# Kernel tuning notes

Hardware: AMD Instinct MI355X
Metric: run time of the kernel (lower is better)

## Reference

```python
import jax, jax.numpy as jnp
import numpy as np

H = 4      # SSM / attn heads (d_model/headdim = 256/64)
WIN = 4    # attention window over bands


def _ln(x, g, b):
    m = jnp.mean(x, -1, keepdims=True)
    v = jnp.mean((x - m) ** 2, -1, keepdims=True)
    return (x - m) * jax.lax.rsqrt(v + 1e-5) * g + b


def setup_inputs() -> dict:
    key = jax.random.key(0)
    ks = jax.random.split(key, 24)
    def rn(i, shape, s=0.05):
        return jax.random.normal(ks[i], shape, jnp.float32) * s
    B, T, K, D = 2, 256, 8, 256
    return {
        "z": rn(0, (B, T, K, D), 1.0),
        "ln1_g": jnp.ones((D,), jnp.float32), "ln1_b": jnp.zeros((D,), jnp.float32),
        "Wx": rn(1, (D, D)), "conv_w": rn(2, (D, 4), 0.3), "Wz": rn(3, (D, D)),
        "Wb": rn(4, (D, H * 128)), "Wc": rn(5, (D, H * 128)), "Wdt": rn(6, (D, H)),
        "dt_bias": rn(7, (H,), 0.5), "A_log": rn(8, (H,), 0.5), "theta": rn(9, (H,), 1.0),
        "D_skip": rn(10, (H,), 1.0), "mimo_U": rn(11, (H, H), 0.5), "mimo_V": rn(12, (H, H), 0.5),
        "Wout": rn(13, (D, D)),
        "ln2_g": jnp.ones((D,), jnp.float32), "ln2_b": jnp.zeros((D,), jnp.float32),
        "attn_in_w": rn(14, (3 * D, D)), "attn_in_b": rn(15, (3 * D,), 0.02),
        "attn_out_w": rn(16, (D, D)), "attn_out_b": jnp.zeros((D,), jnp.float32),
        "ln3_g": jnp.ones((D,), jnp.float32), "ln3_b": jnp.zeros((D,), jnp.float32),
        "Wg": rn(17, (D, 4 * D)), "Wu": rn(18, (D, 4 * D)), "Wd": rn(19, (4 * D, D)),
    }


def _forward(z, ln1_g, ln1_b, Wx, conv_w, Wz, Wb, Wc, Wdt, dt_bias, A_log, theta,
             D_skip, mimo_U, mimo_V, Wout, ln2_g, ln2_b, attn_in_w, attn_in_b,
             attn_out_w, attn_out_b, ln3_g, ln3_b, Wg, Wu, Wd):
    B, T, K, D = z.shape
    P = D // H
    N = Wb.shape[1] // H
    # ---------- (a) intra-band Mamba3 (complex MIMO selective scan) ----------
    u = _ln(z, ln1_g, ln1_b)
    u = jnp.transpose(u, (0, 2, 1, 3)).reshape(B * K, T, D)   # [BK,T,D]
    x = u @ Wx
    # causal depthwise conv1d, kernel 4
    xp = jnp.pad(x, ((0, 0), (3, 0), (0, 0)))
    x = sum(xp[:, k:k + T, :] * conv_w[:, k] for k in range(4))
    x = jax.nn.silu(x)
    xh = x.reshape(B * K, T, H, P)
    Bm = (u @ Wb).reshape(B * K, T, H, N)
    Cm = (u @ Wc).reshape(B * K, T, H, N)
    Mmix = mimo_U @ mimo_V.T                                  # rank-r cross-head coupling
    Bm = jnp.einsum('hg,btgn->bthn', Mmix, Bm)
    dt = jax.nn.softplus(u @ Wdt + dt_bias)                   # [BK,T,H]
    A = -jnp.exp(A_log)                                       # stable real decay
    mag = jnp.exp(dt * A)
    ph = dt * theta                                           # harmonic rotation
    ar, ai = mag * jnp.cos(ph), mag * jnp.sin(ph)
    xs = tuple(jnp.moveaxis(t, 1, 0) for t in (xh, Bm, Cm, dt, ar, ai))
    h0 = jnp.zeros((B * K, H, N, P), x.dtype)

    def step(carry, s):
        h_re, h_im = carry
        xt, bt, ct, dtt, art, ait = s
        dBx = (dtt[:, :, None, None] * bt[:, :, :, None]) * xt[:, :, None, :]
        nr = art[:, :, None, None] * h_re - ait[:, :, None, None] * h_im + dBx
        ni = art[:, :, None, None] * h_im + ait[:, :, None, None] * h_re
        return (nr, ni), jnp.einsum('bhn,bhnp->bhp', ct, nr)   # Re(C . h)

    _, ys = jax.lax.scan(step, (h0, h0), xs)                  # ys: [T,BK,H,P]
    y = jnp.moveaxis(ys, 0, 1) + D_skip[None, None, :, None] * xh
    y = y.reshape(B * K, T, D) * jax.nn.silu(u @ Wz)
    y = y @ Wout
    z = z + jnp.transpose(y.reshape(B, K, T, D), (0, 2, 1, 3))
    # ---------- (b) inter-band windowed attention ----------
    zn = _ln(z, ln2_g, ln2_b).reshape(B * T, K, D)
    qkv = zn @ attn_in_w.T + attn_in_b
    q, k_, v = jnp.split(qkv, 3, axis=-1)
    hd = D // H
    def hs(t):
        return t.reshape(B * T, K // WIN, WIN, H, hd).transpose(0, 1, 3, 2, 4)
    q, k_, v = hs(q), hs(k_), hs(v)
    s = jnp.einsum('mwhqd,mwhkd->mwhqk', q, k_) * jnp.float32(1.0 / np.sqrt(hd))
    a = jax.nn.softmax(s, axis=-1)
    o = jnp.einsum('mwhqk,mwhkd->mwhqd', a, v).transpose(0, 1, 3, 2, 4).reshape(B * T, K, D)
    z = z + (o @ attn_out_w.T + attn_out_b).reshape(B, T, K, D)
    # ---------- (c) SwiGLU FFN ----------
    zf = _ln(z, ln3_g, ln3_b)
    z = z + (jax.nn.silu(zf @ Wg) * (zf @ Wu)) @ Wd
    return z


def reference(z, ln1_g, ln1_b, Wx, conv_w, Wz, Wb, Wc, Wdt, dt_bias, A_log, theta,
              D_skip, mimo_U, mimo_V, Wout, ln2_g, ln2_b, attn_in_w, attn_in_b,
              attn_out_w, attn_out_b, ln3_g, ln3_b, Wg, Wu, Wd):
    return _forward(z, ln1_g, ln1_b, Wx, conv_w, Wz, Wb, Wc, Wdt, dt_bias, A_log,
                    theta, D_skip, mimo_U, mimo_V, Wout, ln2_g, ln2_b, attn_in_w,
                    attn_in_b, attn_out_w, attn_out_b, ln3_g, ln3_b, Wg, Wu, Wd)
```

## Files before the change

### kernel.cpp

```cpp
#include <hip/hip_runtime.h>
#include <hip/hip_bf16.h>
#include <math.h>

typedef __hip_bfloat16 bf16;
typedef __attribute__((ext_vector_type(8))) short s16x8;
typedef __attribute__((ext_vector_type(4))) float f32x4;

__device__ __forceinline__ float siluf(float x) { return x / (1.f + __expf(-x)); }
__device__ __forceinline__ float bits2f(unsigned short u) {
    union { float f; unsigned i; } v; v.i = ((unsigned)u) << 16; return v.f;
}
__device__ __forceinline__ unsigned short f2bits(float f) {
    return (unsigned short)__bfloat16_as_ushort(__float2bfloat16(f));
}

#define KFL 1024
#define OFF_UB   (768*KFL)
#define OFF_DTV  (1280*KFL)
#define OFF_BMB  (1344*KFL)
#define OFF_CMB  (2368*KFL)
#define OFF_ZGB  (3392*KFL)
#define OFF_XB   (3904*KFL)
#define OFF_X2T  (4928*KFL)
#define OFF_P    (5440*KFL)
#define OFF_YGB  (7488*KFL)
#define OFF_Z2   (8000*KFL)
#define OFF_ZFB  (9024*KFL)
#define OFF_GG   OFF_BMB

#define W_BCZX 0
#define W_OUT  393216
#define W_QKV  458752
#define W_AO   655360
#define W_GU   720896
#define W_D    1245184

__global__ __launch_bounds__(256) void prep_ln1_kernel(
    const float* __restrict__ Wx, const float* __restrict__ Wb,
    const float* __restrict__ Wc, const float* __restrict__ Wz,
    const float* __restrict__ Wo, const float* __restrict__ Wqkv,
    const float* __restrict__ Wao, const float* __restrict__ Wg,
    const float* __restrict__ Wu, const float* __restrict__ Wd,
    const float* __restrict__ U, const float* __restrict__ V,
    unsigned short* __restrict__ wout,
    const float* __restrict__ z, const float* __restrict__ g1,
    const float* __restrict__ b1, const float* __restrict__ Wdt,
    const float* __restrict__ dt_bias,
    unsigned short* __restrict__ u, float4* __restrict__ dtv4)
{
    __shared__ __align__(16) float smem[64 * 65];
    int blk = blockIdx.x;
    int tid = threadIdx.x;
    if (blk < 368) {
        if (blk >= 304) {
            int off = blk - 304;
            const float* src; int dst, base;
            if (off < 48) { src = Wqkv; dst = W_QKV; base = off * 4096; }
            else          { src = Wao;  dst = W_AO;  base = (off - 48) * 4096; }
            #pragma unroll
            for (int i = 0; i < 16; i++) {
                int idx = base + tid + i * 256;
                wout[dst + idx] = f2bits(src[idx]);
            }
            return;
        }
        float* lds = smem;
        const float* src; int srcN, n0, sc0, k0, dstoff, dstK, mix = 0, t;
        if (blk < 32)       { t = blk;       src = Wb; srcN = 512;  dstoff = W_BCZX; dstK = 256;
                              n0 = (t >> 2) * 64;        sc0 = 0; k0 = (t & 3) * 64; mix = 1; }
        else if (blk < 64)  { t = blk - 32;  src = Wc; srcN = 512;  dstoff = W_BCZX; dstK = 256;
                              n0 = 512 + (t >> 2) * 64;  sc0 = (t >> 2) * 64; k0 = (t & 3) * 64; }
        else if (blk < 80)  { t = blk - 64;  src = Wz; srcN = 256;  dstoff = W_BCZX; dstK = 256;
                              n0 = 1024 + (t >> 2) * 64; sc0 = (t >> 2) * 64; k0 = (t & 3) * 64; }
        else if (blk < 96)  { t = blk - 80;  src = Wx; srcN = 256;  dstoff = W_BCZX; dstK = 256;
                              n0 = 1280 + (t >> 2) * 64; sc0 = (t >> 2) * 64; k0 = (t & 3) * 64; }
        else if (blk < 112) { t = blk - 96;  src = Wo; srcN = 256;  dstoff = W_OUT;  dstK = 256;
                              n0 = (t >> 2) * 64;        sc0 = n0; k0 = (t & 3) * 64; }
        else if (blk < 176) { t = blk - 112; src = Wg; srcN = 1024; dstoff = W_GU;   dstK = 256;
                              n0 = (t >> 2) * 64;        sc0 = n0; k0 = (t & 3) * 64; }
        else if (blk < 240) { t = blk - 176; src = Wu; srcN = 1024; dstoff = W_GU;   dstK = 256;
                              n0 = 1024 + (t >> 2) * 64; sc0 = (t >> 2) * 64; k0 = (t & 3) * 64; }
        else                { t = blk - 240; src = Wd; srcN = 256;  dstoff = W_D;    dstK = 1024;
                              n0 = (t >> 4) * 64;        sc0 = n0; k0 = (t & 15) * 64; }
        if (mix) {
            int h = n0 >> 7, scol = n0 & 127;
            float mm[4];
            #pragma unroll
            for (int g = 0; g < 4; g++) {
                float s = 0.f;
                #pragma unroll
                for (int j = 0; j < 4; j++) s += U[h * 4 + j] * V[g * 4 + j];
                mm[g] = s;
            }
            #pragma unroll
            for (int i = 0; i < 16; i++) {
                int idx = tid + i * 256;
                int kk = idx >> 6, nn = idx & 63;
                const float* row = src + (size_t)(k0 + kk) * 512 + scol + nn;
                lds[kk * 65 + nn] = mm[0] * row[0] + mm[1] * row[128]
                                  + mm[2] * row[256] + mm[3] * row[384];
            }
        } else {
            #pragma unroll
            for (int i = 0; i < 16; i++) {
                int idx = tid + i * 256;
                int kk = idx >> 6, nn = idx & 63;
                lds[kk * 65 + nn] = src[(size_t)(k0 + kk) * srcN + sc0 + nn];
            }
        }
        __syncthreads();
        #pragma unroll
        for (int i = 0; i < 16; i++) {
            int idx = tid + i * 256;
            int nn = idx >> 6, kk = idx & 63;
            wout[dstoff + (size_t)(n0 + nn) * dstK + k0 + kk] = f2bits(lds[kk * 65 + nn]);
        }
        return;
    }
    int r = blk - 368;
    float* lds = smem;
    float* dts = smem + 4;
    int t = r & 255, bk = r >> 8;
    int b_ = bk >> 3, k = bk & 7;
    int srcr = ((b_ * 256 + t) * 8 + k) * 256;
    int d = tid;
    float x = z[srcr + d];
    float v = x;
    #pragma unroll
    for (int off = 32; off; off >>= 1) v += __shfl_xor(v, off, 64);
    if ((d & 63) == 0) lds[d >> 6] = v;
    __syncthreads();
    float mean = (lds[0] + lds[1] + lds[2] + lds[3]) * (1.f / 256.f);
    __syncthreads();
    float c = x - mean;
    v = c * c;
    #pragma unroll
    for (int off = 32; off; off >>= 1) v += __shfl_xor(v, off, 64);
    if ((d & 63) == 0) lds[d >> 6] = v;
    __syncthreads();
    float var = (lds[0] + lds[1] + lds[2] + lds[3]) * (1.f / 256.f);
    float uval = c * rsqrtf(var + 1e-5f) * g1[d] + b1[d];
    u[r * 256 + d] = f2bits(uval);
    float4 wv = *(const float4*)(Wdt + d * 4);
    float q0 = uval * wv.x, q1 = uval * wv.y, q2 = uval * wv.z, q3 = uval * wv.w;
    #pragma unroll
    for (int off = 32; off; off >>= 1) {
        q0 += __shfl_xor(q0, off, 64);
        q1 += __shfl_xor(q1, off, 64);
        q2 += __shfl_xor(q2, off, 64);
        q3 += __shfl_xor(q3, off, 64);
    }
    if ((d & 63) == 0) {
        int w = d >> 6;
        dts[w * 4 + 0] = q0; dts[w * 4 + 1] = q1;
        dts[w * 4 + 2] = q2; dts[w * 4 + 3] = q3;
    }
    __syncthreads();
    if (d == 0) {
        float dv[4];
        #pragma unroll
        for (int h = 0; h < 4; h++) {
            float xx = dts[h] + dts[4 + h] + dts[8 + h] + dts[12 + h] + dt_bias[h];
            dv[h] = (xx > 20.f) ? xx : log1pf(__expf(xx));
        }
        dtv4[r] = make_float4(dv[0], dv[1], dv[2], dv[3]);
    }
}

__global__ __launch_bounds__(256) void gemm_bczx(
    const unsigned short* __restrict__ A, const unsigned short* __restrict__ Bt,
    unsigned short* __restrict__ bmb, unsigned short* __restrict__ cmb,
    unsigned short* __restrict__ zgb, unsigned short* __restrict__ xb)
{
    __shared__ __align__(16) unsigned short As[128 * 72];
    __shared__ __align__(16) unsigned short Bs[128 * 72];
    const int K = 256;
    int tid = threadIdx.x;
    int n0 = blockIdx.x * 128, m0 = blockIdx.y * 128;
    int w = tid >> 6, l = tid & 63;
    int mwave = (w >> 1) * 64, nwave = (w & 1) * 64;
    f32x4 acc[4][4] = {};
    int srow = tid >> 3, sc = (tid & 7) * 8;
    const unsigned short* Ap = A + (size_t)(m0 + srow) * K + sc;
    const unsigned short* Bp = Bt + (size_t)(n0 + srow) * K + sc;
    int lq = l & 15, lh = l >> 4;
    uint4 a0 = *(const uint4*)(Ap);
    uint4 a1 = *(const uint4*)(Ap + (size_t)32 * K);
    uint4 a2 = *(const uint4*)(Ap + (size_t)64 * K);
    uint4 a3 = *(const uint4*)(Ap + (size_t)96 * K);
    uint4 b0 = *(const uint4*)(Bp);
    uint4 b1 = *(const uint4*)(Bp + (size_t)32 * K);
    uint4 b2 = *(const uint4*)(Bp + (size_t)64 * K);
    uint4 b3 = *(const uint4*)(Bp + (size_t)96 * K);
    for (int k0 = 0; k0 < K; k0 += 64) {
        if (k0) __syncthreads();
        *(uint4*)&As[srow * 72 + sc] = a0;
        *(uint4*)&As[(srow + 32) * 72 + sc] = a1;
        *(uint4*)&As[(srow + 64) * 72 + sc] = a2;
        *(uint4*)&As[(srow + 96) * 72 + sc] = a3;
        *(uint4*)&Bs[srow * 72 + sc] = b0;
        *(uint4*)&Bs[(srow + 32) * 72 + sc] = b1;
        *(uint4*)&Bs[(srow + 64) * 72 + sc] = b2;
        *(uint4*)&Bs[(srow + 96) * 72 + sc] = b3;
        __syncthreads();
        if (k0 + 64 < K) {
            a0 = *(const uint4*)(Ap + k0 + 64);
            a1 = *(const uint4*)(Ap + (size_t)32 * K + k0 + 64);
            a2 = *(const uint4*)(Ap + (size_t)64 * K + k0 + 64);
            a3 = *(const uint4*)(Ap + (size_t)96 * K + k0 + 64);
            b0 = *(const uint4*)(Bp + k0 + 64);
            b1 = *(const uint4*)(Bp + (size_t)32 * K + k0 + 64);
            b2 = *(const uint4*)(Bp + (size_t)64 * K + k0 + 64);
            b3 = *(const uint4*)(Bp + (size_t)96 * K + k0 + 64);
        }
        #pragma unroll
        for (int kk = 0; kk < 2; kk++) {
            int kof = kk * 32 + lh * 8;
            s16x8 bfr[4];
            #pragma unroll
            for (int nf = 0; nf < 4; nf++)
                bfr[nf] = *(const s16x8*)&Bs[(nwave + nf * 16 + lq) * 72 + kof];
            #pragma unroll
            for (int mf = 0; mf < 4; mf++) {
                s16x8 af = *(const s16x8*)&As[(mwave + mf * 16 + lq) * 72 + kof];
                #pragma unroll
                for (int nf = 0; nf < 4; nf++)
                    acc[mf][nf] = __builtin_amdgcn_mfma_f32_16x16x32_bf16(af, bfr[nf], acc[mf][nf], 0, 0, 0);
            }
        }
    }
    #pragma unroll
    for (int mf = 0; mf < 4; mf++) {
        #pragma unroll
        for (int nf = 0; nf < 4; nf++) {
            int n = n0 + nwave + nf * 16 + lq;
            #pragma unroll
            for (int r = 0; r < 4; r++) {
                int m = m0 + mwave + mf * 16 + (l >> 4) * 4 + r;
                float v = acc[mf][nf][r];
                if (n < 512)       bmb[(size_t)m * 512 + n] = f2bits(v);
                else if (n < 1024) cmb[(size_t)m * 512 + (n - 512)] = f2bits(v);
                else if (n < 1280) zgb[(size_t)m * 256 + (n - 1024)] = f2bits(siluf(v));
                else               xb[(size_t)m * 256 + (n - 1280)] = f2bits(v);
            }
        }
    }
}

__global__ __launch_bounds__(256) void s_conv_kernel(
    const unsigned short* __restrict__ cmb, const unsigned short* __restrict__ bmb,
    const float4* __restrict__ dtv4, const float* __restrict__ A_log,
    const float* __restrict__ theta, unsigned short* __restrict__ P,
    const unsigned short* __restrict__ xb, const float* __restrict__ cw,
    unsigned short* __restrict__ x2t)
{
    __shared__ __align__(16) char smem[39936];
    int blk = blockIdx.x;
    int tid = threadIdx.x;
    if (blk >= 192) {
        int c = blk - 192;
        int bhid = c >> 2, tt = c & 3;
        int bk = bhid >> 2, h = bhid & 3;
        int t0 = tt * 64;
        float* tile = (float*)smem;
        #pragma unroll
        for (int i = 0; i < 17; i++) {
            int idx = tid + i * 256;
            if (idx < 67 * 64) {
                int tr = idx >> 6, dd = idx & 63;
                int t = t0 - 3 + tr;
                tile[tr * 65 + dd] = (t >= 0)
                    ? bits2f(xb[(size_t)(bk * 256 + t) * 256 + h * 64 + dd]) : 0.f;
            }
        }
        __syncthreads();
        int wv_ = tid >> 6, lt = tid & 63;
        #pragma unroll 4
        for (int pi = 0; pi < 16; pi++) {
            int p = wv_ * 16 + pi;
            float4 wv = *(const float4*)(cw + (h * 64 + p) * 4);
            float acc = tile[lt * 65 + p] * wv.x + tile[(lt + 1) * 65 + p] * wv.y +
                        tile[(lt + 2) * 65 + p] * wv.z + tile[(lt + 3) * 65 + p] * wv.w;
            x2t[(size_t)(bhid * 64 + p) * 256 + t0 + lt] = f2bits(siluf(acc));
        }
        return;
    }
    int map = blk >> 6;
    int bh = blk & 63;
    int bx = (map == 2) ? 1 : 0;
    int by = (map == 0) ? 0 : 1;
    int bk = bh >> 2, h = bh & 3;
    unsigned short* As = (unsigned short*)smem;
    unsigned short* Bs = As + 128 * 72;
    float* mAs = (float*)(smem + 36864);
    float* phs = mAs + 256;
    float* dss = phs + 256;
    int srow = tid >> 3, sc = (tid & 7) * 8;
    const unsigned short* Ap = cmb + (size_t)(bk * 256 + by * 128 + srow) * 512 + h * 128 + sc;
    const unsigned short* Bp = bmb + (size_t)(bk * 256 + bx * 128 + srow) * 512 + h * 128 + sc;
    uint4 a0 = *(const uint4*)(Ap);
    uint4 a1 = *(const uint4*)(Ap + (size_t)32 * 512);
    uint4 a2 = *(const uint4*)(Ap + (size_t)64 * 512);
    uint4 a3 = *(const uint4*)(Ap + (size_t)96 * 512);
    uint4 b0 = *(const uint4*)(Bp);
    uint4 b1 = *(const uint4*)(Bp + (size_t)32 * 512);
    uint4 b2 = *(const uint4*)(Bp + (size_t)64 * 512);
    uint4 b3 = *(const uint4*)(Bp + (size_t)96 * 512);
    {
        float4 dv = dtv4[bk * 256 + tid];
        float dth = (h == 0) ? dv.x : (h == 1) ? dv.y : (h == 2) ? dv.z : dv.w;
        float Ah = -__expf(A_log[h]);
        float th = theta[h];
        dss[tid] = dth;
        mAs[tid] = dth * Ah;
        phs[tid] = dth * th;
        __syncthreads();
        for (int off = 1; off < 256; off <<= 1) {
            float a = 0.f, p = 0.f;
            int use = (tid >= off);
            if (use) { a = mAs[tid - off]; p = phs[tid - off]; }
            __syncthreads();
            if (use) { mAs[tid] += a; phs[tid] += p; }
            __syncthreads();
        }
    }
    int w = tid >> 6, l = tid & 63;
    int mwave = (w >> 1) * 64, nwave = (w & 1) * 64;
    int lq = l & 15, lh = l >> 4;
    unsigned short* Pout = P + (size_t)bh * 65536;
    f32x4 acc[4][4] = {};
    for (int k0 = 0; k0 < 128; k0 += 64) {
        __syncthreads();
        *(uint4*)&As[srow * 72 + sc] = a0;
        *(uint4*)&As[(srow + 32) * 72 + sc] = a1;
        *(uint4*)&As[(srow + 64) * 72 + sc] = a2;
        *(uint4*)&As[(srow + 96) * 72 + sc] = a3;
        *(uint4*)&Bs[srow * 72 + sc] = b0;
        *(uint4*)&Bs[(srow + 32) * 72 + sc] = b1;
        *(uint4*)&Bs[(srow + 64) * 72 + sc] = b2;
        *(uint4*)&Bs[(srow + 96) * 72 + sc] = b3;
        __syncthreads();
        if (k0 + 64 < 128) {
            a0 = *(const uint4*)(Ap + k0 + 64);
            a1 = *(const uint4*)(Ap + (size_t)32 * 512 + k0 + 64);
            a2 = *(const uint4*)(Ap + (size_t)64 * 512 + k0 + 64);
            a3 = *(const uint4*)(Ap + (size_t)96 * 512 + k0 + 64);
            b0 = *(const uint4*)(Bp + k0 + 64);
            b1 = *(const uint4*)(Bp + (size_t)32 * 512 + k0 + 64);
            b2 = *(const uint4*)(Bp + (size_t)64 * 512 + k0 + 64);
            b3 = *(const uint4*)(Bp + (size_t)96 * 512 + k0 + 64);
        }
        #pragma unroll
        for (int kk = 0; kk < 2; kk++) {
            int kof = kk * 32 + lh * 8;
            s16x8 bfr[4];
            #pragma unroll
            for (int nf = 0; nf < 4; nf++)
                bfr[nf] = *(const s16x8*)&Bs[(nwave + nf * 16 + lq) * 72 + kof];
            #pragma unroll
            for (int mf = 0; mf < 4; mf++) {
                s16x8 af = *(const s16x8*)&As[(mwave + mf * 16 + lq) * 72 + kof];
                #pragma unroll
                for (int nf = 0; nf < 4; nf++)
                    acc[mf][nf] = __builtin_amdgcn_mfma_f32_16x16x32_bf16(af, bfr[nf], acc[mf][nf], 0, 0, 0);
            }
        }
    }
    #pragma unroll
    for (int mf = 0; mf < 4; mf++) {
        float tmv[4], tpv[4]; int tg[4];
        #pragma unroll
        for (int r = 0; r < 4; r++) {
            tg[r] = by * 128 + mwave + mf * 16 + lh * 4 + r;
            tmv[r] = mAs[tg[r]];
            tpv[r] = phs[tg[r]];
        }
        #pragma unroll
        for (int nf = 0; nf < 4; nf++) {
            int s = bx * 128 + nwave + nf * 16 + lq;
            float ms = mAs[s];
            float ps = phs[s];
            float ds = dss[s];
            #pragma unroll
            for (int r = 0; r < 4; r++) {
                float wgt = (s <= tg[r])
                    ? __expf(tmv[r] - ms) * __cosf(tpv[r] - ps) * ds : 0.f;
                Pout[tg[r] * 256 + s] = f2bits(acc[mf][nf][r] * wgt);
            }
        }
    }
}

__global__ __launch_bounds__(256) void gemm_y(
    const unsigned short* __restrict__ P, const unsigned short* __restrict__ x2t,
    const unsigned short* __restrict__ zgb, const float* __restrict__ Dsk,
    unsigned short* __restrict__ ygb)
{
    int by = blockIdx.x, bh = blockIdx.y;
    int bk = bh >> 2, h = bh & 3;
    int tid = threadIdx.x;
    int w = tid >> 6, l = tid & 63;
    int mw = (w >> 1) * 32, nw = (w & 1) * 32;
    int lq = l & 15, lh = l >> 4;
    __shared__ __align__(16) unsigned short As[64 * 72];
    __shared__ __align__(16) unsigned short Bs[64 * 72];
    f32x4 acc[2][2] = {};
    int srow = tid >> 3, sc = (tid & 7) * 8;
    const unsigned short* Ap = P + (size_t)bh * 65536 + (size_t)(by * 64 + srow) * 256 + sc;
    const unsigned short* Bp = x2t + (size_t)bh * 16384 + (size_t)srow * 256 + sc;
    int kmax = (by + 1) * 64; if (kmax > 256) kmax = 256;
    uint4 a0 = *(const uint4*)(Ap);
    uint4 a1 = *(const uint4*)(Ap + (size_t)32 * 256);
    uint4 b0 = *(const uint4*)(Bp);
    uint4 b1 = *(const uint4*)(Bp + (size_t)32 * 256);
    for (int k0 = 0; k0 < kmax; k0 += 64) {
        if (k0) __syncthreads();
        *(uint4*)&As[srow * 72 + sc] = a0;
        *(uint4*)&As[(srow + 32) * 72 + sc] = a1;
        *(uint4*)&Bs[srow * 72 + sc] = b0;
        *(uint4*)&Bs[(srow + 32) * 72 + sc] = b1;
        __syncthreads();
        if (k0 + 64 < kmax) {
            a0 = *(const uint4*)(Ap + k0 + 64);
            a1 = *(const uint4*)(Ap + (size_t)32 * 256 + k0 + 64);
            b0 = *(const uint4*)(Bp + k0 + 64);
            b1 = *(const uint4*)(Bp + (size_t)32 * 256 + k0 + 64);
        }
        #pragma unroll
        for (int kk = 0; kk < 2; kk++) {
            int kof = kk * 32 + lh * 8;
            s16x8 bfr[2];
            #pragma unroll
            for (int nf = 0; nf < 2; nf++)
                bfr[nf] = *(const s16x8*)&Bs[(nw + nf * 16 + lq) * 72 + kof];
            #pragma unroll
            for (int mf = 0; mf < 2; mf++) {
                s16x8 af = *(const s16x8*)&As[(mw + mf * 16 + lq) * 72 + kof];
                #pragma unroll
                for (int nf = 0; nf < 2; nf++)
                    acc[mf][nf] = __builtin_amdgcn_mfma_f32_16x16x32_bf16(af, bfr[nf], acc[mf][nf], 0, 0, 0);
            }
        }
    }
    float dsk = Dsk[h];
    #pragma unroll
    for (int mf = 0; mf < 2; mf++) {
        #pragma unroll
        for (int nf = 0; nf < 2; nf++) {
            int p = nw + nf * 16 + lq;
            #pragma unroll
            for (int r = 0; r < 4; r++) {
                int t = by * 64 + mw + mf * 16 + lh * 4 + r;
                float xv = bits2f(x2t[(size_t)bh * 16384 + p * 256 + t]);
                float zg = bits2f(zgb[(size_t)(bk * 256 + t) * 256 + h * 64 + p]);
                ygb[(size_t)(bk * 256 + t) * 256 + h * 64 + p] =
                    f2bits((acc[mf][nf][r] + dsk * xv) * zg);
            }
        }
    }
}

__global__ __launch_bounds__(256) void mid_kernel(
    const unsigned short* __restrict__ ygb, const unsigned short* __restrict__ wts,
    const float* __restrict__ zin,
    const float* __restrict__ g2, const float* __restrict__ b2,
    const float* __restrict__ qbias, const float* __restrict__ obias,
    const float* __restrict__ g3, const float* __restrict__ b3,
    float* __restrict__ z2, unsigned short* __restrict__ zfb)
{
    __shared__ __align__(16) char smem[64512];
    unsigned short* Bs = (unsigned short*)smem;
    unsigned short* As = (unsigned short*)(smem + 36864);
    unsigned short* zn = (unsigned short*)(smem + 39168);
    float* z1s = (float*)(smem + 47616);
    float (*partS)[4] = (float(*)[4])(smem + 64000);
    float (*partQ)[4] = (float(*)[4])(smem + 64256);
    unsigned short* qk = (unsigned short*)smem;

    const int K = 256;
    int tid = threadIdx.x;
    int m0 = blockIdx.x * 16;
    int w = tid >> 6, l = tid & 63;
    int nw = w * 64;
    int lq = l & 15, lh = l >> 4;
    int srow = tid >> 3, sc = (tid & 7) * 8;

    {
        int rb = m0 + (srow & 15);
        int irow = ((rb >> 11) * 8 + (rb & 7)) * 256 + ((rb >> 3) & 255);
        const unsigned short* Ap = ygb + (size_t)irow * K + sc;
        const unsigned short* Bp = wts + W_OUT + (size_t)srow * K + sc;
        f32x4 acc[4] = {};
        uint4 a0 = *(const uint4*)(Ap);
        uint4 c0 = *(const uint4*)(Bp);
        uint4 c1 = *(const uint4*)(Bp + (size_t)32 * K);
        uint4 c2 = *(const uint4*)(Bp + (size_t)64 * K);
        uint4 c3 = *(const uint4*)(Bp + (size_t)96 * K);
        uint4 c4 = *(const uint4*)(Bp + (size_t)128 * K);
        uint4 c5 = *(const uint4*)(Bp + (size_t)160 * K);
        uint4 c6 = *(const uint4*)(Bp + (size_t)192 * K);
        uint4 c7 = *(const uint4*)(Bp + (size_t)224 * K);
        for (int k0 = 0; k0 < K; k0 += 64) {
            if (k0) __syncthreads();
            if (tid < 128) *(uint4*)&As[srow * 72 + sc] = a0;
            *(uint4*)&Bs[srow * 72 + sc] = c0;
            *(uint4*)&Bs[(srow + 32) * 72 + sc] = c1;
            *(uint4*)&Bs[(srow + 64) * 72 + sc] = c2;
            *(uint4*)&Bs[(srow + 96) * 72 + sc] = c3;
            *(uint4*)&Bs[(srow + 128) * 72 + sc] = c4;
            *(uint4*)&Bs[(srow + 160) * 72 + sc] = c5;
            *(uint4*)&Bs[(srow + 192) * 72 + sc] = c6;
            *(uint4*)&Bs[(srow + 224) * 72 + sc] = c7;
            __syncthreads();
            if (k0 + 64 < K) {
                a0 = *(const uint4*)(Ap + k0 + 64);
                c0 = *(const uint4*)(Bp + k0 + 64);
                c1 = *(const uint4*)(Bp + (size_t)32 * K + k0 + 64);
                c2 = *(const uint4*)(Bp + (size_t)64 * K + k0 + 64);
                c3 = *(const uint4*)(Bp + (size_t)96 * K + k0 + 64);
                c4 = *(const uint4*)(Bp + (size_t)128 * K + k0 + 64);
                c5 = *(const uint4*)(Bp + (size_t)160 * K + k0 + 64);
                c6 = *(const uint4*)(Bp + (size_t)192 * K + k0 + 64);
                c7 = *(const uint4*)(Bp + (size_t)224 * K + k0 + 64);
            }
            #pragma unroll
            for (int kk = 0; kk < 2; kk++) {
                int kof = kk * 32 + lh * 8;
                s16x8 af = *(const s16x8*)&As[lq * 72 + kof];
                #pragma unroll
                for (int nf = 0; nf < 4; nf++) {
                    s16x8 bf = *(const s16x8*)&Bs[(nw + nf * 16 + lq) * 72 + kof];
                    acc[nf] = __builtin_amdgcn_mfma_f32_16x16x32_bf16(af, bf, acc[nf], 0, 0, 0);
                }
            }
        }
        #pragma unroll
        for (int r = 0; r < 4; r++) {
            int row = lh * 4 + r;
            float s = 0.f, q = 0.f;
            #pragma unroll
            for (int nf = 0; nf < 4; nf++) {
                float v = acc[nf][r] + zin[(size_t)(m0 + row) * 256 + nw + nf * 16 + lq];
                acc[nf][r] = v;
                s += v; q += v * v;
            }
            #pragma unroll
            for (int off = 1; off < 16; off <<= 1) {
                s += __shfl_xor(s, off, 64);
                q += __shfl_xor(q, off, 64);
            }
            if (lq == 0) { partS[row][w] = s; partQ[row][w] = q; }
        }
        __syncthreads();
        float gv[4], bbv[4];
        #pragma unroll
        for (int nf = 0; nf < 4; nf++) {
            gv[nf] = g2[nw + nf * 16 + lq];
            bbv[nf] = b2[nw + nf * 16 + lq];
        }
        #pragma unroll
        for (int r = 0; r < 4; r++) {
            int row = lh * 4 + r;
            float sum = partS[row][0] + partS[row][1] + partS[row][2] + partS[row][3];
            float sq  = partQ[row][0] + partQ[row][1] + partQ[row][2] + partQ[row][3];
            float mean = sum * (1.f / 256.f);
            float var = sq * (1.f / 256.f) - mean * mean;
            float rstd = rsqrtf(var + 1e-5f);
            #pragma unroll
            for (int nf = 0; nf < 4; nf++) {
                int n = nw + nf * 16 + lq;
                float v = acc[nf][r];
                z1s[row * 256 + n] = v;
                zn[row * 264 + n] = f2bits((v - mean) * rstd * gv[nf] + bbv[nf]);
            }
        }
    }

    f32x4 aq0[4] = {}, aq1[4] = {}, aq2[4] = {};
#define QKV_PASS(PIDX, AQ) do { \
    const unsigned short* Bp2 = wts + W_QKV + (size_t)((PIDX) * 256 + srow) * 256 + sc; \
    uint4 d0 = *(const uint4*)(Bp2); \
    uint4 d1 = *(const uint4*)(Bp2 + (size_t)32 * 256); \
    uint4 d2 = *(const uint4*)(Bp2 + (size_t)64 * 256); \
    uint4 d3 = *(const uint4*)(Bp2 + (size_t)96 * 256); \
    uint4 d4 = *(const uint4*)(Bp2 + (size_t)128 * 256); \
    uint4 d5 = *(const uint4*)(Bp2 + (size_t)160 * 256); \
    uint4 d6 = *(const uint4*)(Bp2 + (size_t)192 * 256); \
    uint4 d7 = *(const uint4*)(Bp2 + (size_t)224 * 256); \
    for (int k0 = 0; k0 < 256; k0 += 64) { \
        __syncthreads(); \
        *(uint4*)&Bs[srow * 72 + sc] = d0; \
        *(uint4*)&Bs[(srow + 32) * 72 + sc] = d1; \
        *(uint4*)&Bs[(srow + 64) * 72 + sc] = d2; \
        *(uint4*)&Bs[(srow + 96) * 72 + sc] = d3; \
        *(uint4*)&Bs[(srow + 128) * 72 + sc] = d4; \
        *(uint4*)&Bs[(srow + 160) * 72 + sc] = d5; \
        *(uint4*)&Bs[(srow + 192) * 72 + sc] = d6; \
        *(uint4*)&Bs[(srow + 224) * 72 + sc] = d7; \
        __syncthreads(); \
        if (k0 + 64 < 256) { \
            d0 = *(const uint4*)(Bp2 + k0 + 64); \
            d1 = *(const uint4*)(Bp2 + (size_t)32 * 256 + k0 + 64); \
            d2 = *(const uint4*)(Bp2 + (size_t)64 * 256 + k0 + 64); \
            d3 = *(const uint4*)(Bp2 + (size_t)96 * 256 + k0 + 64); \
            d4 = *(const uint4*)(Bp2 + (size_t)128 * 256 + k0 + 64); \
            d5 = *(const uint4*)(Bp2 + (size_t)160 * 256 + k0 + 64); \
            d6 = *(const uint4*)(Bp2 + (size_t)192 * 256 + k0 + 64); \
            d7 = *(const uint4*)(Bp2 + (size_t)224 * 256 + k0 + 64); \
        } \
        _Pragma("unroll") \
        for (int kk = 0; kk < 2; kk++) { \
            int kof = kk * 32 + lh * 8; \
            s16x8 af = *(const s16x8*)&zn[lq * 264 + k0 + kof]; \
            _Pragma("unroll") \
            for (int nf = 0; nf < 4; nf++) { \
                s16x8 bf = *(const s16x8*)&Bs[(nw + nf * 16 + lq) * 72 + kof]; \
                AQ[nf] = __builtin_amdgcn_mfma_f32_16x16x32_bf16(af, bf, AQ[nf], 0, 0, 0); \
            } \
        } \
    } \
} while (0)
    QKV_PASS(0, aq0);
    QKV_PASS(1, aq1);
    QKV_PASS(2, aq2);
#undef QKV_PASS

    __syncthreads();
#define QKV_STORE(PIDX, AQ) do { \
    _Pragma("unroll") \
    for (int nf = 0; nf < 4; nf++) { \
        int n = (PIDX) * 256 + nw + nf * 16 + lq; \
        float bb = qbias[n]; \
        _Pragma("unroll") \
        for (int r = 0; r < 4; r++) \
            qk[(lh * 4 + r) * 776 + n] = f2bits(AQ[nf][r] + bb); \
    } \
} while (0)
    QKV_STORE(0, aq0);
    QKV_STORE(1, aq1);
    QKV_STORE(2, aq2);
#undef QKV_STORE
    __syncthreads();
    {
        int hh = w;
        int d = l;
        #pragma unroll
        for (int w4 = 0; w4 < 4; w4++) {
            int r0 = w4 * 4;
            float qv[4], kv[4], vv[4];
            #pragma unroll
            for (int j = 0; j < 4; j++) {
                qv[j] = bits2f(qk[(r0 + j) * 776 + hh * 64 + d]);
                kv[j] = bits2f(qk[(r0 + j) * 776 + 256 + hh * 64 + d]);
                vv[j] = bits2f(qk[(r0 + j) * 776 + 512 + hh * 64 + d]);
            }
            float sc_[4][4];
            #pragma unroll
            for (int qi = 0; qi < 4; qi++)
                #pragma unroll
                for (int ki = 0; ki < 4; ki++) {
                    float v = qv[qi] * kv[ki];
                    #pragma unroll
                    for (int off = 32; off; off >>= 1) v += __shfl_xor(v, off, 64);
                    sc_[qi][ki] = v * 0.125f;
                }
            #pragma unroll
            for (int qi = 0; qi < 4; qi++) {
                float mx = fmaxf(fmaxf(sc_[qi][0], sc_[qi][1]), fmaxf(sc_[qi][2], sc_[qi][3]));
                float e0 = __expf(sc_[qi][0] - mx), e1 = __expf(sc_[qi][1] - mx);
                float e2 = __expf(sc_[qi][2] - mx), e3 = __expf(sc_[qi][3] - mx);
                float inv = 1.f / (e0 + e1 + e2 + e3);
                float ov = (e0 * vv[0] + e1 * vv[1] + e2 * vv[2] + e3 * vv[3]) * inv;
                zn[(r0 + qi) * 264 + hh * 64 + d] = f2bits(ov);
            }
        }
    }

    {
        f32x4 ac4[4] = {};
        const unsigned short* Bp4 = wts + W_AO + (size_t)srow * K + sc;
        uint4 c0 = *(const uint4*)(Bp4);
        uint4 c1 = *(const uint4*)(Bp4 + (size_t)32 * K);
        uint4 c2 = *(const uint4*)(Bp4 + (size_t)64 * K);
        uint4 c3 = *(const uint4*)(Bp4 + (size_t)96 * K);
        uint4 c4 = *(const uint4*)(Bp4 + (size_t)128 * K);
        uint4 c5 = *(const uint4*)(Bp4 + (size_t)160 * K);
        uint4 c6 = *(const uint4*)(Bp4 + (size_t)192 * K);
        uint4 c7 = *(const uint4*)(Bp4 + (size_t)224 * K);
        for (int k0 = 0; k0 < K; k0 += 64) {
            __syncthreads();
            *(uint4*)&Bs[srow * 72 + sc] = c0;
            *(uint4*)&Bs[(srow + 32) * 72 + sc] = c1;
            *(uint4*)&Bs[(srow + 64) * 72 + sc] = c2;
            *(uint4*)&Bs[(srow + 96) * 72 + sc] = c3;
            *(uint4*)&Bs[(srow + 128) * 72 + sc] = c4;
            *(uint4*)&Bs[(srow + 160) * 72 + sc] = c5;
            *(uint4*)&Bs[(srow + 192) * 72 + sc] = c6;
            *(uint4*)&Bs[(srow + 224) * 72 + sc] = c7;
            __syncthreads();
            if (k0 + 64 < K) {
                c0 = *(const uint4*)(Bp4 + k0 + 64);
                c1 = *(const uint4*)(Bp4 + (size_t)32 * K + k0 + 64);
                c2 = *(const uint4*)(Bp4 + (size_t)64 * K + k0 + 64);
                c3 = *(const uint4*)(Bp4 + (size_t)96 * K + k0 + 64);
                c4 = *(const uint4*)(Bp4 + (size_t)128 * K + k0 + 64);
                c5 = *(const uint4*)(Bp4 + (size_t)160 * K + k0 + 64);
                c6 = *(const uint4*)(Bp4 + (size_t)192 * K + k0 + 64);
                c7 = *(const uint4*)(Bp4 + (size_t)224 * K + k0 + 64);
            }
            #pragma unroll
            for (int kk = 0; kk < 2; kk++) {
                int kof = kk * 32 + lh * 8;
                s16x8 af = *(const s16x8*)&zn[lq * 264 + k0 + kof];
                #pragma unroll
                for (int nf = 0; nf < 4; nf++) {
                    s16x8 bf = *(const s16x8*)&Bs[(nw + nf * 16 + lq) * 72 + kof];
                    ac4[nf] = __builtin_amdgcn_mfma_f32_16x16x32_bf16(af, bf, ac4[nf], 0, 0, 0);
                }
            }
        }
        float bv[4], gv[4], bbv[4];
        #pragma unroll
        for (int nf = 0; nf < 4; nf++) {
            int n = nw + nf * 16 + lq;
            bv[nf] = obias[n];
            gv[nf] = g3[n];
            bbv[nf] = b3[n];
        }
        #pragma unroll
        for (int r = 0; r < 4; r++) {
            int row = lh * 4 + r;
            float s = 0.f, q = 0.f;
            #pragma unroll
            for (int nf = 0; nf < 4; nf++) {
                float v = ac4[nf][r] + bv[nf] + z1s[row * 256 + nw + nf * 16 + lq];
                ac4[nf][r] = v;
                s += v; q += v * v;
            }
            #pragma unroll
            for (int off = 1; off < 16; off <<= 1) {
                s += __shfl_xor(s, off, 64);
                q += __shfl_xor(q, off, 64);
            }
            if (lq == 0) { partS[row][w] = s; partQ[row][w] = q; }
        }
        __syncthreads();
        #pragma unroll
        for (int r = 0; r < 4; r++) {
            int row = lh * 4 + r;
            float sum = partS[row][0] + partS[row][1] + partS[row][2] + partS[row][3];
            float sq  = partQ[row][0] + partQ[row][1] + partQ[row][2] + partQ[row][3];
            float mean = sum * (1.f / 256.f);
            float var = sq * (1.f / 256.f) - mean * mean;
            float rstd = rsqrtf(var + 1e-5f);
            size_t ro = (size_t)(m0 + row) * 256;
            #pragma unroll
            for (int nf = 0; nf < 4; nf++) {
                int n = nw + nf * 16 + lq;
                float v = ac4[nf][r];
                z2[ro + n] = v;
                zfb[ro + n] = f2bits((v - mean) * rstd * gv[nf] + bbv[nf]);
            }
        }
    }
}

__global__ __launch_bounds__(256) void gemm_gu2(
    const unsigned short* __restrict__ A, const unsigned short* __restrict__ Wgu,
    unsigned short* __restrict__ gg)
{
    const int K = 256;
    __shared__ __align__(16) unsigned short As[128 * 72];
    __shared__ __align__(16) unsigned short Bgs[64 * 72];
    __shared__ __align__(16) unsigned short Bus[64 * 72];
    int tid = threadIdx.x;
    int n0 = blockIdx.x * 64, m0 = blockIdx.y * 128;
    int w = tid >> 6, l = tid & 63;
    int mwave = (w >> 1) * 64, nwave = (w & 1) * 32;
    int lq = l & 15, lh = l >> 4;
    f32x4 ag[4][2] = {}, au[4][2] = {};
    int srow = tid >> 3, sc = (tid & 7) * 8;
    const unsigned short* Ap = A + (size_t)(m0 + srow) * K + sc;
    const unsigned short* Bgp = Wgu + (size_t)(n0 + srow) * K + sc;
    const unsigned short* Bup = Wgu + (size_t)(1024 + n0 + srow) * K + sc;
    uint4 a0 = *(const uint4*)(Ap);
    uint4 a1 = *(const uint4*)(Ap + (size_t)32 * K);
    uint4 a2 = *(const uint4*)(Ap + (size_t)64 * K);
    uint4 a3 = *(const uint4*)(Ap + (size_t)96 * K);
    uint4 bg0 = *(const uint4*)(Bgp);
    uint4 bg1 = *(const uint4*)(Bgp + (size_t)32 * K);
    uint4 bu0 = *(const uint4*)(Bup);
    uint4 bu1 = *(const uint4*)(Bup + (size_t)32 * K);
    for (int k0 = 0; k0 < K; k0 += 64) {
        if (k0) __syncthreads();
        *(uint4*)&As[srow * 72 + sc] = a0;
        *(uint4*)&As[(srow + 32) * 72 + sc] = a1;
        *(uint4*)&As[(srow + 64) * 72 + sc] = a2;
        *(uint4*)&As[(srow + 96) * 72 + sc] = a3;
        *(uint4*)&Bgs[srow * 72 + sc] = bg0;
        *(uint4*)&Bgs[(srow + 32) * 72 + sc] = bg1;
        *(uint4*)&Bus[srow * 72 + sc] = bu0;
        *(uint4*)&Bus[(srow + 32) * 72 + sc] = bu1;
        __syncthreads();
        if (k0 + 64 < K) {
            a0 = *(const uint4*)(Ap + k0 + 64);
            a1 = *(const uint4*)(Ap + (size_t)32 * K + k0 + 64);
            a2 = *(const uint4*)(Ap + (size_t)64 * K + k0 + 64);
            a3 = *(const uint4*)(Ap + (size_t)96 * K + k0 + 64);
            bg0 = *(const uint4*)(Bgp + k0 + 64);
            bg1 = *(const uint4*)(Bgp + (size_t)32 * K + k0 + 64);
            bu0 = *(const uint4*)(Bup + k0 + 64);
            bu1 = *(const uint4*)(Bup + (size_t)32 * K + k0 + 64);
        }
        #pragma unroll
        for (int kk = 0; kk < 2; kk++) {
            int kof = kk * 32 + lh * 8;
            s16x8 bgr[2], bur[2];
            #pragma unroll
            for (int nf = 0; nf < 2; nf++) {
                bgr[nf] = *(const s16x8*)&Bgs[(nwave + nf * 16 + lq) * 72 + kof];
                bur[nf] = *(const s16x8*)&Bus[(nwave + nf * 16 + lq) * 72 + kof];
            }
            #pragma unroll
            for (int mf = 0; mf < 4; mf++) {
                s16x8 af = *(const s16x8*)&As[(mwave + mf * 16 + lq) * 72 + kof];
                #pragma unroll
                for (int nf = 0; nf < 2; nf++) {
                    ag[mf][nf] = __builtin_amdgcn_mfma_f32_16x16x32_bf16(af, bgr[nf], ag[mf][nf], 0, 0, 0);
                    au[mf][nf] = __builtin_amdgcn_mfma_f32_16x16x32_bf16(af, bur[nf], au[mf][nf], 0, 0, 0);
                }
            }
        }
    }
    #pragma unroll
    for (int mf = 0; mf < 4; mf++) {
        #pragma unroll
        for (int nf = 0; nf < 2; nf++) {
            int n = n0 + nwave + nf * 16 + lq;
            #pragma unroll
            for (int r = 0; r < 4; r++) {
                int m = m0 + mwave + mf * 16 + lh * 4 + r;
                gg[(size_t)m * 1024 + n] = f2bits(siluf(ag[mf][nf][r]) * au[mf][nf][r]);
            }
        }
    }
}

__global__ __launch_bounds__(256) void gemm_d2(
    const unsigned short* __restrict__ gg, const unsigned short* __restrict__ Bt,
    const float* __restrict__ resid, float* __restrict__ out)
{
    __shared__ __align__(16) unsigned short As[64 * 72];
    __shared__ __align__(16) unsigned short Bs[64 * 72];
    const int K = 1024, N = 256;
    int tid = threadIdx.x;
    int n0 = blockIdx.x * 64, m0 = blockIdx.y * 64;
    int w = tid >> 6, l = tid & 63;
    int mw = (w >> 1) * 32, nw = (w & 1) * 32;
    f32x4 acc[2][2] = {};
    int srow = tid >> 3, sc = (tid & 7) * 8;
    const unsigned short* Ap = gg + (size_t)(m0 + srow) * K + sc;
    const unsigned short* Bp = Bt + (size_t)(n0 + srow) * K + sc;
    int lq = l & 15, lh = l >> 4;
    uint4 a0 = *(const uint4*)(Ap);
    uint4 a1 = *(const uint4*)(Ap + (size_t)32 * K);
    uint4 b0 = *(const uint4*)(Bp);
    uint4 b1 = *(const uint4*)(Bp + (size_t)32 * K);
    for (int k0 = 0; k0 < K; k0 += 64) {
        if (k0) __syncthreads();
        *(uint4*)&As[srow * 72 + sc] = a0;
        *(uint4*)&As[(srow + 32) * 72 + sc] = a1;
        *(uint4*)&Bs[srow * 72 + sc] = b0;
        *(uint4*)&Bs[(srow + 32) * 72 + sc] = b1;
        __syncthreads();
        if (k0 + 64 < K) {
            a0 = *(const uint4*)(Ap + k0 + 64);
            a1 = *(const uint4*)(Ap + (size_t)32 * K + k0 + 64);
            b0 = *(const uint4*)(Bp + k0 + 64);
            b1 = *(const uint4*)(Bp + (size_t)32 * K + k0 + 64);
        }
        #pragma unroll
        for (int kk = 0; kk < 2; kk++) {
            int kof = kk * 32 + lh * 8;
            s16x8 bfr[2];
            #pragma unroll
            for (int nf = 0; nf < 2; nf++)
                bfr[nf] = *(const s16x8*)&Bs[(nw + nf * 16 + lq) * 72 + kof];
            #pragma unroll
            for (int mf = 0; mf < 2; mf++) {
                s16x8 af = *(const s16x8*)&As[(mw + mf * 16 + lq) * 72 + kof];
                #pragma unroll
                for (int nf = 0; nf < 2; nf++)
                    acc[mf][nf] = __builtin_amdgcn_mfma_f32_16x16x32_bf16(af, bfr[nf], acc[mf][nf], 0, 0, 0);
            }
        }
    }
    #pragma unroll
    for (int mf = 0; mf < 2; mf++) {
        #pragma unroll
        for (int nf = 0; nf < 2; nf++) {
            int n = n0 + nw + nf * 16 + lq;
            #pragma unroll
            for (int r = 0; r < 4; r++) {
                int m = m0 + mw + mf * 16 + lh * 4 + r;
                out[(size_t)m * N + n] = acc[mf][nf][r] + resid[(size_t)m * N + n];
            }
        }
    }
}

extern "C" void kernel_launch(void* const* d_in, const int* in_sizes, int n_in,
                              void* d_out, int out_size, void* d_ws, size_t ws_size,
                              hipStream_t stream)
{
    const float* z         = (const float*)d_in[0];
    const float* ln1_g     = (const float*)d_in[1];
    const float* ln1_b     = (const float*)d_in[2];
    const float* Wx        = (const float*)d_in[3];
    const float* conv_w    = (const float*)d_in[4];
    const float* Wz        = (const float*)d_in[5];
    const float* Wb        = (const float*)d_in[6];
    const float* Wc        = (const float*)d_in[7];
    const float* Wdt       = (const float*)d_in[8];
    const float* dt_bias   = (const float*)d_in[9];
    const float* A_log     = (const float*)d_in[10];
    const float* theta     = (const float*)d_in[11];
    const float* D_skip    = (const float*)d_in[12];
    const float* mimo_U    = (const float*)d_in[13];
    const float* mimo_V    = (const float*)d_in[14];
    const float* Wout      = (const float*)d_in[15];
    const float* ln2_g     = (const float*)d_in[16];
    const float* ln2_b     = (const float*)d_in[17];
    const float* attn_in_w = (const float*)d_in[18];
    const float* attn_in_b = (const float*)d_in[19];
    const float* attn_out_w= (const float*)d_in[20];
    const float* attn_out_b= (const float*)d_in[21];
    const float* ln3_g     = (const float*)d_in[22];
    const float* ln3_b     = (const float*)d_in[23];
    const float* Wg        = (const float*)d_in[24];
    const float* Wu        = (const float*)d_in[25];
    const float* Wd        = (const float*)d_in[26];

    float* W = (float*)d_ws;
    unsigned short* wts = (unsigned short*)W;
    unsigned short* ub  = (unsigned short*)(W + OFF_UB);
    float4* dtv4        = (float4*)(W + OFF_DTV);
    unsigned short* bmb = (unsigned short*)(W + OFF_BMB);
    unsigned short* cmb = (unsigned short*)(W + OFF_CMB);
    unsigned short* zgb = (unsigned short*)(W + OFF_ZGB);
    unsigned short* xb  = (unsigned short*)(W + OFF_XB);
    unsigned short* x2t = (unsigned short*)(W + OFF_X2T);
    unsigned short* pbuf= (unsigned short*)(W + OFF_P);
    unsigned short* ygb = (unsigned short*)(W + OFF_YGB);
    float* z2           = W + OFF_Z2;
    unsigned short* zfb = (unsigned short*)(W + OFF_ZFB);
    unsigned short* gg  = (unsigned short*)(W + OFF_GG);

    prep_ln1_kernel<<<4464, 256, 0, stream>>>(
        Wx, Wb, Wc, Wz, Wout, attn_in_w, attn_out_w, Wg, Wu, Wd, mimo_U, mimo_V,
        wts, z, ln1_g, ln1_b, Wdt, dt_bias, ub, dtv4);
    gemm_bczx<<<dim3(12, 32), 256, 0, stream>>>(ub, wts + W_BCZX, bmb, cmb, zgb, xb);
    s_conv_kernel<<<448, 256, 0, stream>>>(cmb, bmb, dtv4, A_log, theta, pbuf,
                                           xb, conv_w, x2t);
    gemm_y<<<dim3(4, 64), 256, 0, stream>>>(pbuf, x2t, zgb, D_skip, ygb);
    mid_kernel<<<256, 256, 0, stream>>>(ygb, wts, z, ln2_g, ln2_b,
                                        attn_in_b, attn_out_b, ln3_g, ln3_b,
                                        z2, zfb);
    gemm_gu2<<<dim3(16, 32), 256, 0, stream>>>(zfb, wts + W_GU, gg);
    gemm_d2<<<dim3(4, 64), 256, 0, stream>>>(gg, wts + W_D, z2, (float*)d_out);
}
```

Baseline: 198.6 us.

## Load MFMA fragments directly from global memory, removing LDS staging in all GEMMs

Every GEMM-like loop (projection, scan score, scan output, out-proj/QKV, gate/up, down) now loads bf16 MFMA operand fragments straight from global memory into registers instead of staging tiles through shared memory with barriers. This removes LDS writes, reads and __syncthreads, and shrinks the shared-memory footprint, which may raise occupancy. In exchange, each wave rereads operands that other waves in the block also load, relying on L1/L2 caches. The loads are 16-byte strided rows, so they may be less coalesced.

New measurement: 239.5 us. +20.6%, slower.

```diff
diff --git a/kernel.cpp b/kernel.cpp
--- a/kernel.cpp
+++ b/kernel.cpp
@@ -172,62 +172,29 @@
     unsigned short* __restrict__ bmb, unsigned short* __restrict__ cmb,
     unsigned short* __restrict__ zgb, unsigned short* __restrict__ xb)
 {
-    __shared__ __align__(16) unsigned short As[128 * 72];
-    __shared__ __align__(16) unsigned short Bs[128 * 72];
     const int K = 256;
     int tid = threadIdx.x;
     int n0 = blockIdx.x * 128, m0 = blockIdx.y * 128;
     int w = tid >> 6, l = tid & 63;
     int mwave = (w >> 1) * 64, nwave = (w & 1) * 64;
+    int lq = l & 15, lh = l >> 4;
     f32x4 acc[4][4] = {};
-    int srow = tid >> 3, sc = (tid & 7) * 8;
-    const unsigned short* Ap = A + (size_t)(m0 + srow) * K + sc;
-    const unsigned short* Bp = Bt + (size_t)(n0 + srow) * K + sc;
-    int lq = l & 15, lh = l >> 4;
-    uint4 a0 = *(const uint4*)(Ap);
-    uint4 a1 = *(const uint4*)(Ap + (size_t)32 * K);
-    uint4 a2 = *(const uint4*)(Ap + (size_t)64 * K);
-    uint4 a3 = *(const uint4*)(Ap + (size_t)96 * K);
-    uint4 b0 = *(const uint4*)(Bp);
-    uint4 b1 = *(const uint4*)(Bp + (size_t)32 * K);
-    uint4 b2 = *(const uint4*)(Bp + (size_t)64 * K);
-    uint4 b3 = *(const uint4*)(Bp + (size_t)96 * K);
-    for (int k0 = 0; k0 < K; k0 += 64) {
-        if (k0) __syncthreads();
-        *(uint4*)&As[srow * 72 + sc] = a0;
-        *(uint4*)&As[(srow + 32) * 72 + sc] = a1;
-        *(uint4*)&As[(srow + 64) * 72 + sc] = a2;
-        *(uint4*)&As[(srow + 96) * 72 + sc] = a3;
-        *(uint4*)&Bs[srow * 72 + sc] = b0;
-        *(uint4*)&Bs[(srow + 32) * 72 + sc] = b1;
-        *(uint4*)&Bs[(srow + 64) * 72 + sc] = b2;
-        *(uint4*)&Bs[(srow + 96) * 72 + sc] = b3;
-        __syncthreads();
-        if (k0 + 64 < K) {
-            a0 = *(const uint4*)(Ap + k0 + 64);
-            a1 = *(const uint4*)(Ap + (size_t)32 * K + k0 + 64);
-            a2 = *(const uint4*)(Ap + (size_t)64 * K + k0 + 64);
-            a3 = *(const uint4*)(Ap + (size_t)96 * K + k0 + 64);
-            b0 = *(const uint4*)(Bp + k0 + 64);
-            b1 = *(const uint4*)(Bp + (size_t)32 * K + k0 + 64);
-            b2 = *(const uint4*)(Bp + (size_t)64 * K + k0 + 64);
-            b3 = *(const uint4*)(Bp + (size_t)96 * K + k0 + 64);
-        }
-        #pragma unroll
-        for (int kk = 0; kk < 2; kk++) {
-            int kof = kk * 32 + lh * 8;
-            s16x8 bfr[4];
+    const unsigned short* Ab = A + (size_t)(m0 + mwave + lq) * K + lh * 8;
+    const unsigned short* Bb = Bt + (size_t)(n0 + nwave + lq) * K + lh * 8;
+    #pragma unroll 2
+    for (int k = 0; k < K; k += 32) {
+        s16x8 af[4], bf[4];
+        #pragma unroll
+        for (int mf = 0; mf < 4; mf++)
+            af[mf] = *(const s16x8*)(Ab + (size_t)mf * 16 * K + k);
+        #pragma unroll
+        for (int nf = 0; nf < 4; nf++)
+            bf[nf] = *(const s16x8*)(Bb + (size_t)nf * 16 * K + k);
+        #pragma unroll
+        for (int mf = 0; mf < 4; mf++)
             #pragma unroll
             for (int nf = 0; nf < 4; nf++)
-                bfr[nf] = *(const s16x8*)&Bs[(nwave + nf * 16 + lq) * 72 + kof];
-            #pragma unroll
-            for (int mf = 0; mf < 4; mf++) {
-                s16x8 af = *(const s16x8*)&As[(mwave + mf * 16 + lq) * 72 + kof];
-                #pragma unroll
-                for (int nf = 0; nf < 4; nf++)
-                    acc[mf][nf] = __builtin_amdgcn_mfma_f32_16x16x32_bf16(af, bfr[nf], acc[mf][nf], 0, 0, 0);
-            }
-        }
+                acc[mf][nf] = __builtin_amdgcn_mfma_f32_16x16x32_bf16(af[mf], bf[nf], acc[mf][nf], 0, 0, 0);
     }
     #pragma unroll
     for (int mf = 0; mf < 4; mf++) {
@@ -236,7 +203,7 @@
             int n = n0 + nwave + nf * 16 + lq;
             #pragma unroll
             for (int r = 0; r < 4; r++) {
-                int m = m0 + mwave + mf * 16 + (l >> 4) * 4 + r;
+                int m = m0 + mwave + mf * 16 + lh * 4 + r;
                 float v = acc[mf][nf][r];
                 if (n < 512)       bmb[(size_t)m * 512 + n] = f2bits(v);
                 else if (n < 1024) cmb[(size_t)m * 512 + (n - 512)] = f2bits(v);
@@ -254,7 +221,7 @@
     const unsigned short* __restrict__ xb, const float* __restrict__ cw,
     unsigned short* __restrict__ x2t)
 {
-    __shared__ __align__(16) char smem[39936];
+    __shared__ __align__(16) char smem[17424];
     int blk = blockIdx.x;
     int tid = threadIdx.x;
     if (blk >= 192) {
@@ -290,22 +257,9 @@
     int bx = (map == 2) ? 1 : 0;
     int by = (map == 0) ? 0 : 1;
     int bk = bh >> 2, h = bh & 3;
-    unsigned short* As = (unsigned short*)smem;
-    unsigned short* Bs = As + 128 * 72;
-    float* mAs = (float*)(smem + 36864);
+    float* mAs = (float*)smem;
     float* phs = mAs + 256;
     float* dss = phs + 256;
-    int srow = tid >> 3, sc = (tid & 7) * 8;
-    const unsigned short* Ap = cmb + (size_t)(bk * 256 + by * 128 + srow) * 512 + h * 128 + sc;
-    const unsigned short* Bp = bmb + (size_t)(bk * 256 + bx * 128 + srow) * 512 + h * 128 + sc;
-    uint4 a0 = *(const uint4*)(Ap);
-    uint4 a1 = *(const uint4*)(Ap + (size_t)32 * 512);
-    uint4 a2 = *(const uint4*)(Ap + (size_t)64 * 512);
-    uint4 a3 = *(const uint4*)(Ap + (size_t)96 * 512);
-    uint4 b0 = *(const uint4*)(Bp);
-    uint4 b1 = *(const uint4*)(Bp + (size_t)32 * 512);
-    uint4 b2 = *(const uint4*)(Bp + (size_t)64 * 512);
-    uint4 b3 = *(const uint4*)(Bp + (size_t)96 * 512);
     {
         float4 dv = dtv4[bk * 256 + tid];
         float dth = (h == 0) ? dv.x : (h == 1) ? dv.y : (h == 2) ? dv.z : dv.w;
@@ -329,42 +283,22 @@
     int lq = l & 15, lh = l >> 4;
     unsigned short* Pout = P + (size_t)bh * 65536;
     f32x4 acc[4][4] = {};
-    for (int k0 = 0; k0 < 128; k0 += 64) {
-        __syncthreads();
-        *(uint4*)&As[srow * 72 + sc] = a0;
-        *(uint4*)&As[(srow + 32) * 72 + sc] = a1;
-        *(uint4*)&As[(srow + 64) * 72 + sc] = a2;
-        *(uint4*)&As[(srow + 96) * 72 + sc] = a3;
-        *(uint4*)&Bs[srow * 72 + sc] = b0;
-        *(uint4*)&Bs[(srow + 32) * 72 + sc] = b1;
-        *(uint4*)&Bs[(srow + 64) * 72 + sc] = b2;
-        *(uint4*)&Bs[(srow + 96) * 72 + sc] = b3;
-        __syncthreads();
-        if (k0 + 64 < 128) {
-            a0 = *(const uint4*)(Ap + k0 + 64);
-            a1 = *(const uint4*)(Ap + (size_t)32 * 512 + k0 + 64);
-            a2 = *(const uint4*)(Ap + (size_t)64 * 512 + k0 + 64);
-            a3 = *(const uint4*)(Ap + (size_t)96 * 512 + k0 + 64);
-            b0 = *(const uint4*)(Bp + k0 + 64);
-            b1 = *(const uint4*)(Bp + (size_t)32 * 512 + k0 + 64);
-            b2 = *(const uint4*)(Bp + (size_t)64 * 512 + k0 + 64);
-            b3 = *(const uint4*)(Bp + (size_t)96 * 512 + k0 + 64);
-        }
-        #pragma unroll
-        for (int kk = 0; kk < 2; kk++) {
-            int kof = kk * 32 + lh * 8;
-            s16x8 bfr[4];
+    const unsigned short* Ab = cmb + (size_t)(bk * 256 + by * 128 + mwave + lq) * 512 + h * 128 + lh * 8;
+    const unsigned short* Bb = bmb + (size_t)(bk * 256 + bx * 128 + nwave + lq) * 512 + h * 128 + lh * 8;
+    #pragma unroll
+    for (int k = 0; k < 128; k += 32) {
+        s16x8 af[4], bf[4];
+        #pragma unroll
+        for (int mf = 0; mf < 4; mf++)
+            af[mf] = *(const s16x8*)(Ab + (size_t)mf * 16 * 512 + k);
+        #pragma unroll
+        for (int nf = 0; nf < 4; nf++)
+            bf[nf] = *(const s16x8*)(Bb + (size_t)nf * 16 * 512 + k);
+        #pragma unroll
+        for (int mf = 0; mf < 4; mf++)
             #pragma unroll
             for (int nf = 0; nf < 4; nf++)
-                bfr[nf] = *(const s16x8*)&Bs[(nwave + nf * 16 + lq) * 72 + kof];
-            #pragma unroll
-            for (int mf = 0; mf < 4; mf++) {
-                s16x8 af = *(const s16x8*)&As[(mwave + mf * 16 + lq) * 72 + kof];
-                #pragma unroll
-                for (int nf = 0; nf < 4; nf++)
-                    acc[mf][nf] = __builtin_amdgcn_mfma_f32_16x16x32_bf16(af, bfr[nf], acc[mf][nf], 0, 0, 0);
-            }
-        }
+                acc[mf][nf] = __builtin_amdgcn_mfma_f32_16x16x32_bf16(af[mf], bf[nf], acc[mf][nf], 0, 0, 0);
     }
     #pragma unroll
     for (int mf = 0; mf < 4; mf++) {
@@ -402,45 +336,24 @@
     int w = tid >> 6, l = tid & 63;
     int mw = (w >> 1) * 32, nw = (w & 1) * 32;
     int lq = l & 15, lh = l >> 4;
-    __shared__ __align__(16) unsigned short As[64 * 72];
-    __shared__ __align__(16) unsigned short Bs[64 * 72];
     f32x4 acc[2][2] = {};
-    int srow = tid >> 3, sc = (tid & 7) * 8;
-    const unsigned short* Ap = P + (size_t)bh * 65536 + (size_t)(by * 64 + srow) * 256 + sc;
-    const unsigned short* Bp = x2t + (size_t)bh * 16384 + (size_t)srow * 256 + sc;
     int kmax = (by + 1) * 64; if (kmax > 256) kmax = 256;
-    uint4 a0 = *(const uint4*)(Ap);
-    uint4 a1 = *(const uint4*)(Ap + (size_t)32 * 256);
-    uint4 b0 = *(const uint4*)(Bp);
-    uint4 b1 = *(const uint4*)(Bp + (size_t)32 * 256);
-    for (int k0 = 0; k0 < kmax; k0 += 64) {
-        if (k0) __syncthreads();
-        *(uint4*)&As[srow * 72 + sc] = a0;
-        *(uint4*)&As[(srow + 32) * 72 + sc] = a1;
-        *(uint4*)&Bs[srow * 72 + sc] = b0;
-        *(uint4*)&Bs[(srow + 32) * 72 + sc] = b1;
-        __syncthreads();
-        if (k0 + 64 < kmax) {
-            a0 = *(const uint4*)(Ap + k0 + 64);
-            a1 = *(const uint4*)(Ap + (size_t)32 * 256 + k0 + 64);
-            b0 = *(const uint4*)(Bp + k0 + 64);
-            b1 = *(const uint4*)(Bp + (size_t)32 * 256 + k0 + 64);
-        }
-        #pragma unroll
-        for (int kk = 0; kk < 2; kk++) {
-            int kof = kk * 32 + lh * 8;
-            s16x8 bfr[2];
+    const unsigned short* Ab = P + (size_t)bh * 65536 + (size_t)(by * 64 + mw + lq) * 256 + lh * 8;
+    const unsigned short* Bb = x2t + (size_t)bh * 16384 + (size_t)(nw + lq) * 256 + lh * 8;
+    #pragma unroll 4
+    for (int k = 0; k < kmax; k += 32) {
+        s16x8 af[2], bf[2];
+        #pragma unroll
+        for (int mf = 0; mf < 2; mf++)
+            af[mf] = *(const s16x8*)(Ab + (size_t)mf * 16 * 256 + k);
+        #pragma unroll
+        for (int nf = 0; nf < 2; nf++)
+            bf[nf] = *(const s16x8*)(Bb + (size_t)nf * 16 * 256 + k);
+        #pragma unroll
+        for (int mf = 0; mf < 2; mf++)
             #pragma unroll
             for (int nf = 0; nf < 2; nf++)
-                bfr[nf] = *(const s16x8*)&Bs[(nw + nf * 16 + lq) * 72 + kof];
-            #pragma unroll
-            for (int mf = 0; mf < 2; mf++) {
-                s16x8 af = *(const s16x8*)&As[(mw + mf * 16 + lq) * 72 + kof];
-                #pragma unroll
-                for (int nf = 0; nf < 2; nf++)
-                    acc[mf][nf] = __builtin_amdgcn_mfma_f32_16x16x32_bf16(af, bfr[nf], acc[mf][nf], 0, 0, 0);
-            }
-        }
+                acc[mf][nf] = __builtin_amdgcn_mfma_f32_16x16x32_bf16(af[mf], bf[nf], acc[mf][nf], 0, 0, 0);
     }
     float dsk = Dsk[h];
     #pragma unroll
@@ -468,14 +381,12 @@
     const float* __restrict__ g3, const float* __restrict__ b3,
     float* __restrict__ z2, unsigned short* __restrict__ zfb)
 {
-    __shared__ __align__(16) char smem[64512];
-    unsigned short* Bs = (unsigned short*)smem;
-    unsigned short* As = (unsigned short*)(smem + 36864);
-    unsigned short* zn = (unsigned short*)(smem + 39168);
-    float* z1s = (float*)(smem + 47616);
-    float (*partS)[4] = (float(*)[4])(smem + 64000);
-    float (*partQ)[4] = (float(*)[4])(smem + 64256);
-    unsigned short* qk = (unsigned short*)smem;
+    __shared__ __align__(16) char smem[50688];
+    unsigned short* zn = (unsigned short*)smem;
+    float* z1s = (float*)(smem + 8448);
+    float (*partS)[4] = (float(*)[4])(smem + 24832);
+    float (*partQ)[4] = (float(*)[4])(smem + 25088);
+    unsigned short* qk = (unsigned short*)(smem + 25344);
 
     const int K = 256;
     int tid = threadIdx.x;
@@ -483,55 +394,20 @@
     int w = tid >> 6, l = tid & 63;
     int nw = w * 64;
     int lq = l & 15, lh = l >> 4;
-    int srow = tid >> 3, sc = (tid & 7) * 8;
 
     {
-        int rb = m0 + (srow & 15);
+        int rb = m0 + lq;
         int irow = ((rb >> 11) * 8 + (rb & 7)) * 256 + ((rb >> 3) & 255);
-        const unsigned short* Ap = ygb + (size_t)irow * K + sc;
-        const unsigned short* Bp = wts + W_OUT + (size_t)srow * K + sc;
+        const unsigned short* Ab = ygb + (size_t)irow * K + lh * 8;
+        const unsigned short* Bb = wts + W_OUT + (size_t)(nw + lq) * K + lh * 8;
         f32x4 acc[4] = {};
-        uint4 a0 = *(const uint4*)(Ap);
-        uint4 c0 = *(const uint4*)(Bp);
-        uint4 c1 = *(const uint4*)(Bp + (size_t)32 * K);
-        uint4 c2 = *(const uint4*)(Bp + (size_t)64 * K);
-        uint4 c3 = *(const uint4*)(Bp + (size_t)96 * K);
-        uint4 c4 = *(const uint4*)(Bp + (size_t)128 * K);
-        uint4 c5 = *(const uint4*)(Bp + (size_t)160 * K);
-        uint4 c6 = *(const uint4*)(Bp + (size_t)192 * K);
-        uint4 c7 = *(const uint4*)(Bp + (size_t)224 * K);
-        for (int k0 = 0; k0 < K; k0 += 64) {
-            if (k0) __syncthreads();
-            if (tid < 128) *(uint4*)&As[srow * 72 + sc] = a0;
-            *(uint4*)&Bs[srow * 72 + sc] = c0;
-            *(uint4*)&Bs[(srow + 32) * 72 + sc] = c1;
-            *(uint4*)&Bs[(srow + 64) * 72 + sc] = c2;
-            *(uint4*)&Bs[(srow + 96) * 72 + sc] = c3;
-            *(uint4*)&Bs[(srow + 128) * 72 + sc] = c4;
-            *(uint4*)&Bs[(srow + 160) * 72 + sc] = c5;
-            *(uint4*)&Bs[(srow + 192) * 72 + sc] = c6;
-            *(uint4*)&Bs[(srow + 224) * 72 + sc] = c7;
-            __syncthreads();
-            if (k0 + 64 < K) {
-                a0 = *(const uint4*)(Ap + k0 + 64);
-                c0 = *(const uint4*)(Bp + k0 + 64);
-                c1 = *(const uint4*)(Bp + (size_t)32 * K + k0 + 64);
-                c2 = *(const uint4*)(Bp + (size_t)64 * K + k0 + 64);
-                c3 = *(const uint4*)(Bp + (size_t)96 * K + k0 + 64);
-                c4 = *(const uint4*)(Bp + (size_t)128 * K + k0 + 64);
-                c5 = *(const uint4*)(Bp + (size_t)160 * K + k0 + 64);
-                c6 = *(const uint4*)(Bp + (size_t)192 * K + k0 + 64);
-                c7 = *(const uint4*)(Bp + (size_t)224 * K + k0 + 64);
-            }
-            #pragma unroll
-            for (int kk = 0; kk < 2; kk++) {
-                int kof = kk * 32 + lh * 8;
-                s16x8 af = *(const s16x8*)&As[lq * 72 + kof];
-                #pragma unroll
-                for (int nf = 0; nf < 4; nf++) {
-                    s16x8 bf = *(const s16x8*)&Bs[(nw + nf * 16 + lq) * 72 + kof];
-                    acc[nf] = __builtin_amdgcn_mfma_f32_16x16x32_bf16(af, bf, acc[nf], 0, 0, 0);
-                }
+        #pragma unroll 2
+        for (int k = 0; k < K; k += 32) {
+            s16x8 af = *(const s16x8*)(Ab + k);
+            #pragma unroll
+            for (int nf = 0; nf < 4; nf++) {
+                s16x8 bf = *(const s16x8*)(Bb + (size_t)nf * 16 * K + k);
+                acc[nf] = __builtin_amdgcn_mfma_f32_16x16x32_bf16(af, bf, acc[nf], 0, 0, 0);
             }
         }
         #pragma unroll
@@ -575,57 +451,28 @@
             }
         }
     }
+    __syncthreads();
 
     f32x4 aq0[4] = {}, aq1[4] = {}, aq2[4] = {};
-#define QKV_PASS(PIDX, AQ) do { \
-    const unsigned short* Bp2 = wts + W_QKV + (size_t)((PIDX) * 256 + srow) * 256 + sc; \
-    uint4 d0 = *(const uint4*)(Bp2); \
-    uint4 d1 = *(const uint4*)(Bp2 + (size_t)32 * 256); \
-    uint4 d2 = *(const uint4*)(Bp2 + (size_t)64 * 256); \
-    uint4 d3 = *(const uint4*)(Bp2 + (size_t)96 * 256); \
-    uint4 d4 = *(const uint4*)(Bp2 + (size_t)128 * 256); \
-    uint4 d5 = *(const uint4*)(Bp2 + (size_t)160 * 256); \
-    uint4 d6 = *(const uint4*)(Bp2 + (size_t)192 * 256); \
-    uint4 d7 = *(const uint4*)(Bp2 + (size_t)224 * 256); \
-    for (int k0 = 0; k0 < 256; k0 += 64) { \
-        __syncthreads(); \
-        *(uint4*)&Bs[srow * 72 + sc] = d0; \
-        *(uint4*)&Bs[(srow + 32) * 72 + sc] = d1; \
-        *(uint4*)&Bs[(srow + 64) * 72 + sc] = d2; \
-        *(uint4*)&Bs[(srow + 96) * 72 + sc] = d3; \
-        *(uint4*)&Bs[(srow + 128) * 72 + sc] = d4; \
-        *(uint4*)&Bs[(srow + 160) * 72 + sc] = d5; \
-        *(uint4*)&Bs[(srow + 192) * 72 + sc] = d6; \
-        *(uint4*)&Bs[(srow + 224) * 72 + sc] = d7; \
-        __syncthreads(); \
-        if (k0 + 64 < 256) { \
-            d0 = *(const uint4*)(Bp2 + k0 + 64); \
-            d1 = *(const uint4*)(Bp2 + (size_t)32 * 256 + k0 + 64); \
-            d2 = *(const uint4*)(Bp2 + (size_t)64 * 256 + k0 + 64); \
-            d3 = *(const uint4*)(Bp2 + (size_t)96 * 256 + k0 + 64); \
-            d4 = *(const uint4*)(Bp2 + (size_t)128 * 256 + k0 + 64); \
-            d5 = *(const uint4*)(Bp2 + (size_t)160 * 256 + k0 + 64); \
-            d6 = *(const uint4*)(Bp2 + (size_t)192 * 256 + k0 + 64); \
-            d7 = *(const uint4*)(Bp2 + (size_t)224 * 256 + k0 + 64); \
-        } \
-        _Pragma("unroll") \
-        for (int kk = 0; kk < 2; kk++) { \
-            int kof = kk * 32 + lh * 8; \
-            s16x8 af = *(const s16x8*)&zn[lq * 264 + k0 + kof]; \
-            _Pragma("unroll") \
-            for (int nf = 0; nf < 4; nf++) { \
-                s16x8 bf = *(const s16x8*)&Bs[(nw + nf * 16 + lq) * 72 + kof]; \
-                AQ[nf] = __builtin_amdgcn_mfma_f32_16x16x32_bf16(af, bf, AQ[nf], 0, 0, 0); \
-            } \
-        } \
-    } \
-} while (0)
-    QKV_PASS(0, aq0);
-    QKV_PASS(1, aq1);
-    QKV_PASS(2, aq2);
-#undef QKV_PASS
-
-    __syncthreads();
+    {
+        const unsigned short* B0 = wts + W_QKV + (size_t)(nw + lq) * K + lh * 8;
+        const unsigned short* B1 = B0 + (size_t)256 * K;
+        const unsigned short* B2 = B0 + (size_t)512 * K;
+        #pragma unroll 2
+        for (int k = 0; k < K; k += 32) {
+            s16x8 af = *(const s16x8*)&zn[lq * 264 + k + lh * 8];
+            #pragma unroll
+            for (int nf = 0; nf < 4; nf++) {
+                s16x8 b0 = *(const s16x8*)(B0 + (size_t)nf * 16 * K + k);
+                aq0[nf] = __builtin_amdgcn_mfma_f32_16x16x32_bf16(af, b0, aq0[nf], 0, 0, 0);
+                s16x8 b1 = *(const s16x8*)(B1 + (size_t)nf * 16 * K + k);
+                aq1[nf] = __builtin_amdgcn_mfma_f32_16x16x32_bf16(af, b1, aq1[nf], 0, 0, 0);
+                s16x8 b2 = *(const s16x8*)(B2 + (size_t)nf * 16 * K + k);
+                aq2[nf] = __builtin_amdgcn_mfma_f32_16x16x32_bf16(af, b2, aq2[nf], 0, 0, 0);
+            }
+        }
+    }
+
 #define QKV_STORE(PIDX, AQ) do { \
     _Pragma("unroll") \
     for (int nf = 0; nf < 4; nf++) { \
@@ -675,48 +522,18 @@
             }
         }
     }
+    __syncthreads();
 
     {
         f32x4 ac4[4] = {};
-        const unsigned short* Bp4 = wts + W_AO + (size_t)srow * K + sc;
-        uint4 c0 = *(const uint4*)(Bp4);
-        uint4 c1 = *(const uint4*)(Bp4 + (size_t)32 * K);
-        uint4 c2 = *(const uint4*)(Bp4 + (size_t)64 * K);
-        uint4 c3 = *(const uint4*)(Bp4 + (size_t)96 * K);
-        uint4 c4 = *(const uint4*)(Bp4 + (size_t)128 * K);
-        uint4 c5 = *(const uint4*)(Bp4 + (size_t)160 * K);
-        uint4 c6 = *(const uint4*)(Bp4 + (size_t)192 * K);
-        uint4 c7 = *(const uint4*)(Bp4 + (size_t)224 * K);
-        for (int k0 = 0; k0 < K; k0 += 64) {
-            __syncthreads();
-            *(uint4*)&Bs[srow * 72 + sc] = c0;
-            *(uint4*)&Bs[(srow + 32) * 72 + sc] = c1;
-            *(uint4*)&Bs[(srow + 64) * 72 + sc] = c2;
-            *(uint4*)&Bs[(srow + 96) * 72 + sc] = c3;
-            *(uint4*)&Bs[(srow + 128) * 72 + sc] = c4;
-            *(uint4*)&Bs[(srow + 160) * 72 + sc] = c5;
-            *(uint4*)&Bs[(srow + 192) * 72 + sc] = c6;
-            *(uint4*)&Bs[(srow + 224) * 72 + sc] = c7;
-            __syncthreads();
-            if (k0 + 64 < K) {
-                c0 = *(const uint4*)(Bp4 + k0 + 64);
-                c1 = *(const uint4*)(Bp4 + (size_t)32 * K + k0 + 64);
-                c2 = *(const uint4*)(Bp4 + (size_t)64 * K + k0 + 64);
-                c3 = *(const uint4*)(Bp4 + (size_t)96 * K + k0 + 64);
-                c4 = *(const uint4*)(Bp4 + (size_t)128 * K + k0 + 64);
-                c5 = *(const uint4*)(Bp4 + (size_t)160 * K + k0 + 64);
-                c6 = *(const uint4*)(Bp4 + (size_t)192 * K + k0 + 64);
-                c7 = *(const uint4*)(Bp4 + (size_t)224 * K + k0 + 64);
-            }
-            #pragma unroll
-            for (int kk = 0; kk < 2; kk++) {
-                int kof = kk * 32 + lh * 8;
-                s16x8 af = *(const s16x8*)&zn[lq * 264 + k0 + kof];
-                #pragma unroll
-                for (int nf = 0; nf < 4; nf++) {
-                    s16x8 bf = *(const s16x8*)&Bs[(nw + nf * 16 + lq) * 72 + kof];
-                    ac4[nf] = __builtin_amdgcn_mfma_f32_16x16x32_bf16(af, bf, ac4[nf], 0, 0, 0);
-                }
+        const unsigned short* Bb = wts + W_AO + (size_t)(nw + lq) * K + lh * 8;
+        #pragma unroll 2
+        for (int k = 0; k < K; k += 32) {
+            s16x8 af = *(const s16x8*)&zn[lq * 264 + k + lh * 8];
+            #pragma unroll
+            for (int nf = 0; nf < 4; nf++) {
+                s16x8 bf = *(const s16x8*)(Bb + (size_t)nf * 16 * K + k);
+                ac4[nf] = __builtin_amdgcn_mfma_f32_16x16x32_bf16(af, bf, ac4[nf], 0, 0, 0);
             }
         }
         float bv[4], gv[4], bbv[4];
@@ -770,67 +587,33 @@
     unsigned short* __restrict__ gg)
 {
     const int K = 256;
-    __shared__ __align__(16) unsigned short As[128 * 72];
-    __shared__ __align__(16) unsigned short Bgs[64 * 72];
-    __shared__ __align__(16) unsigned short Bus[64 * 72];
     int tid = threadIdx.x;
     int n0 = blockIdx.x * 64, m0 = blockIdx.y * 128;
     int w = tid >> 6, l = tid & 63;
     int mwave = (w >> 1) * 64, nwave = (w & 1) * 32;
     int lq = l & 15, lh = l >> 4;
     f32x4 ag[4][2] = {}, au[4][2] = {};
-    int srow = tid >> 3, sc = (tid & 7) * 8;
-    const unsigned short* Ap = A + (size_t)(m0 + srow) * K + sc;
-    const unsigned short* Bgp = Wgu + (size_t)(n0 + srow) * K + sc;
-    const unsigned short* Bup = Wgu + (size_t)(1024 + n0 + srow) * K + sc;
-    uint4 a0 = *(const uint4*)(Ap);
-    uint4 a1 = *(const uint4*)(Ap + (size_t)32 * K);
-    uint4 a2 = *(const uint4*)(Ap + (size_t)64 * K);
-    uint4 a3 = *(const uint4*)(Ap + (size_t)96 * K);
-    uint4 bg0 = *(const uint4*)(Bgp);
-    uint4 bg1 = *(const uint4*)(Bgp + (size_t)32 * K);
-    uint4 bu0 = *(const uint4*)(Bup);
-    uint4 bu1 = *(const uint4*)(Bup + (size_t)32 * K);
-    for (int k0 = 0; k0 < K; k0 += 64) {
-        if (k0) __syncthreads();
-        *(uint4*)&As[srow * 72 + sc] = a0;
-        *(uint4*)&As[(srow + 32) * 72 + sc] = a1;
-        *(uint4*)&As[(srow + 64) * 72 + sc] = a2;
-        *(uint4*)&As[(srow + 96) * 72 + sc] = a3;
-        *(uint4*)&Bgs[srow * 72 + sc] = bg0;
-        *(uint4*)&Bgs[(srow + 32) * 72 + sc] = bg1;
-        *(uint4*)&Bus[srow * 72 + sc] = bu0;
-        *(uint4*)&Bus[(srow + 32) * 72 + sc] = bu1;
-        __syncthreads();
-        if (k0 + 64 < K) {
-            a0 = *(const uint4*)(Ap + k0 + 64);
-            a1 = *(const uint4*)(Ap + (size_t)32 * K + k0 + 64);
-            a2 = *(const uint4*)(Ap + (size_t)64 * K + k0 + 64);
-            a3 = *(const uint4*)(Ap + (size_t)96 * K + k0 + 64);
-            bg0 = *(const uint4*)(Bgp + k0 + 64);
-            bg1 = *(const uint4*)(Bgp + (size_t)32 * K + k0 + 64);
-            bu0 = *(const uint4*)(Bup + k0 + 64);
-            bu1 = *(const uint4*)(Bup + (size_t)32 * K + k0 + 64);
-        }
-        #pragma unroll
-        for (int kk = 0; kk < 2; kk++) {
-            int kof = kk * 32 + lh * 8;
-            s16x8 bgr[2], bur[2];
+    const unsigned short* Ab = A + (size_t)(m0 + mwave + lq) * K + lh * 8;
+    const unsigned short* Bg = Wgu + (size_t)(n0 + nwave + lq) * K + lh * 8;
+    const unsigned short* Bu = Wgu + (size_t)(1024 + n0 + nwave + lq) * K + lh * 8;
+    #pragma unroll 2
+    for (int k = 0; k < K; k += 32) {
+        s16x8 af[4], bgf[2], buf_[2];
+        #pragma unroll
+        for (int mf = 0; mf < 4; mf++)
+            af[mf] = *(const s16x8*)(Ab + (size_t)mf * 16 * K + k);
+        #pragma unroll
+        for (int nf = 0; nf < 2; nf++) {
+            bgf[nf] = *(const s16x8*)(Bg + (size_t)nf * 16 * K + k);
+            buf_[nf] = *(const s16x8*)(Bu + (size_t)nf * 16 * K + k);
+        }
+        #pragma unroll
+        for (int mf = 0; mf < 4; mf++)
             #pragma unroll
             for (int nf = 0; nf < 2; nf++) {
-                bgr[nf] = *(const s16x8*)&Bgs[(nwave + nf * 16 + lq) * 72 + kof];
-                bur[nf] = *(const s16x8*)&Bus[(nwave + nf * 16 + lq) * 72 + kof];
-            }
-            #pragma unroll
-            for (int mf = 0; mf < 4; mf++) {
-                s16x8 af = *(const s16x8*)&As[(mwave + mf * 16 + lq) * 72 + kof];
-                #pragma unroll
-                for (int nf = 0; nf < 2; nf++) {
-                    ag[mf][nf] = __builtin_amdgcn_mfma_f32_16x16x32_bf16(af, bgr[nf], ag[mf][nf], 0, 0, 0);
-                    au[mf][nf] = __builtin_amdgcn_mfma_f32_16x16x32_bf16(af, bur[nf], au[mf][nf], 0, 0, 0);
-                }
-            }
-        }
+                ag[mf][nf] = __builtin_amdgcn_mfma_f32_16x16x32_bf16(af[mf], bgf[nf], ag[mf][nf], 0, 0, 0);
+                au[mf][nf] = __builtin_amdgcn_mfma_f32_16x16x32_bf16(af[mf], buf_[nf], au[mf][nf], 0, 0, 0);
+            }
     }
     #pragma unroll
     for (int mf = 0; mf < 4; mf++) {
@@ -850,50 +633,29 @@
     const unsigned short* __restrict__ gg, const unsigned short* __restrict__ Bt,
     const float* __restrict__ resid, float* __restrict__ out)
 {
-    __shared__ __align__(16) unsigned short As[64 * 72];
-    __shared__ __align__(16) unsigned short Bs[64 * 72];
     const int K = 1024, N = 256;
     int tid = threadIdx.x;
     int n0 = blockIdx.x * 64, m0 = blockIdx.y * 64;
     int w = tid >> 6, l = tid & 63;
     int mw = (w >> 1) * 32, nw = (w & 1) * 32;
+    int lq = l & 15, lh = l >> 4;
     f32x4 acc[2][2] = {};
-    int srow = tid >> 3, sc = (tid & 7) * 8;
-    const unsigned short* Ap = gg + (size_t)(m0 + srow) * K + sc;
-    const unsigned short* Bp = Bt + (size_t)(n0 + srow) * K + sc;
-    int lq = l & 15, lh = l >> 4;
-    uint4 a0 = *(const uint4*)(Ap);
-    uint4 a1 = *(const uint4*)(Ap + (size_t)32 * K);
-    uint4 b0 = *(const uint4*)(Bp);
-    uint4 b1 = *(const uint4*)(Bp + (size_t)32 * K);
-    for (int k0 = 0; k0 < K; k0 += 64) {
-        if (k0) __syncthreads();
-        *(uint4*)&As[srow * 72 + sc] = a0;
-        *(uint4*)&As[(srow + 32) * 72 + sc] = a1;
-        *(uint4*)&Bs[srow * 72 + sc] = b0;
-        *(uint4*)&Bs[(srow + 32) * 72 + sc] = b1;
-        __syncthreads();
-        if (k0 + 64 < K) {
-            a0 = *(const uint4*)(Ap + k0 + 64);
-            a1 = *(const uint4*)(Ap + (size_t)32 * K + k0 + 64);
-            b0 = *(const uint4*)(Bp + k0 + 64);
-            b1 = *(const uint4*)(Bp + (size_t)32 * K + k0 + 64);
-        }
-        #pragma unroll
-        for (int kk = 0; kk < 2; kk++) {
-            int kof = kk * 32 + lh * 8;
-            s16x8 bfr[2];
+    const unsigned short* Ab = gg + (size_t)(m0 + mw + lq) * K + lh * 8;
+    const unsigned short* Bb = Bt + (size_t)(n0 + nw + lq) * K + lh * 8;
+    #pragma unroll 4
+    for (int k = 0; k < K; k += 32) {
+        s16x8 af[2], bf[2];
+        #pragma unroll
+        for (int mf = 0; mf < 2; mf++)
+            af[mf] = *(const s16x8*)(Ab + (size_t)mf * 16 * K + k);
+        #pragma unroll
+        for (int nf = 0; nf < 2; nf++)
+            bf[nf] = *(const s16x8*)(Bb + (size_t)nf * 16 * K + k);
+        #pragma unroll
+        for (int mf = 0; mf < 2; mf++)
             #pragma unroll
             for (int nf = 0; nf < 2; nf++)
-                bfr[nf] = *(const s16x8*)&Bs[(nw + nf * 16 + lq) * 72 + kof];
-            #pragma unroll
-            for (int mf = 0; mf < 2; mf++) {
-                s16x8 af = *(const s16x8*)&As[(mw + mf * 16 + lq) * 72 + kof];
-                #pragma unroll
-                for (int nf = 0; nf < 2; nf++)
-                    acc[mf][nf] = __builtin_amdgcn_mfma_f32_16x16x32_bf16(af, bfr[nf], acc[mf][nf], 0, 0, 0);
-            }
-        }
+                acc[mf][nf] = __builtin_amdgcn_mfma_f32_16x16x32_bf16(af[mf], bf[nf], acc[mf][nf], 0, 0, 0);
     }
     #pragma unroll
     for (int mf = 0; mf < 2; mf++) {
```
